# Optimization experiments

Hardware: AMD Instinct MI355X
Metric: run time of the kernel (lower is better)

The kernel has to match this reference:

```python
import jax, jax.numpy as jnp
import numpy as np

N_HEAD = 16
SPARSITY_K = 64


def _apply_rope(x):
    # x: [B, H, T, D]
    D = x.shape[-1]
    T = x.shape[-2]
    freqs = 1.0 / (10000.0 ** (jnp.arange(0, D, 2, dtype=jnp.float32) / D))  # [D/2]
    angles = jnp.arange(T, dtype=jnp.float32)[:, None] * freqs[None, :]      # [T, D/2]
    cos, sin = jnp.cos(angles), jnp.sin(angles)
    xe, xo = x[..., ::2], x[..., 1::2]
    re = xe * cos - xo * sin
    ro = xe * sin + xo * cos
    return jnp.stack([re, ro], axis=-1).reshape(x.shape)


def _sparse_mask(route_weights, T, k):
    # Per head h, per query t: keep positions j<=t whose route score is among
    # the top-k of route_weights[h, 0:t+1] (tie-break by smaller index, like topk).
    s = route_weights[:, :T]                      # [H, T]
    idx = jnp.arange(T)
    # G[h, jp, j] = 1 if position jp beats position j in the top-k ordering
    G = (s[:, :, None] > s[:, None, :]) | ((s[:, :, None] == s[:, None, :]) & (idx[:, None] < idx[None, :]))
    rank = jnp.cumsum(G.astype(jnp.int32), axis=1)  # rank[h, t, j] = #{jp<=t beating j}
    causal = idx[None, :, None] >= idx[None, None, :]  # j <= t
    return causal & (rank < k)                    # [H, T, T] bool


def reference(x, W_attn, b_attn, W_proj, b_proj, route_weights):
    B, T, C = x.shape
    H = N_HEAD
    D = C // H
    qkv = x @ W_attn + b_attn                     # [B, T, 3C]
    q, k, v = jnp.split(qkv, 3, axis=-1)

    def heads(t):
        return t.reshape(B, T, H, D).transpose(0, 2, 1, 3)  # [B, H, T, D]

    q, k, v = heads(q), heads(k), heads(v)
    q = _apply_rope(q)
    k = _apply_rope(k)

    scores = jnp.einsum('bhtd,bhsd->bhts', q, k) / jnp.sqrt(jnp.float32(D))
    mask = _sparse_mask(route_weights, T, SPARSITY_K)       # [H, T, T]
    scores = jnp.where(mask[None], scores, -jnp.inf)
    attn = jax.nn.softmax(scores, axis=-1)                  # dropout off (eval mode)
    out = jnp.einsum('bhts,bhsd->bhtd', attn, v)
    out = out.transpose(0, 2, 1, 3).reshape(B, T, C)
    return out @ W_proj + b_proj


def setup_inputs() -> dict:
    key = jax.random.key(0)
    ks = jax.random.split(key, 6)
    B, T, C, H = 2, 2048, 2048, 16
    return {
        'x': jax.random.normal(ks[0], (B, T, C), dtype=jnp.float32),
        'W_attn': jax.random.normal(ks[1], (C, 3 * C), dtype=jnp.float32) * 0.02,
        'b_attn': jnp.zeros((3 * C,), dtype=jnp.float32),
        'W_proj': jax.random.normal(ks[2], (C, C), dtype=jnp.float32) * 0.02,
        'b_proj': jnp.zeros((C,), dtype=jnp.float32),
        'route_weights': jax.random.normal(ks[3], (H, T), dtype=jnp.float32) * 0.02,
    }
```

## Files before the change

### kernel.cpp

```cpp
#include <hip/hip_runtime.h>
#include <stdint.h>

#define B_ 2
#define T_ 2048
#define C_ 2048
#define H_ 16
#define D_ 128
#define KSP 64
#define C3 6144

typedef __attribute__((ext_vector_type(4))) float f32x4;
typedef __attribute__((ext_vector_type(8))) _Float16 f16x8;
typedef __attribute__((ext_vector_type(4))) _Float16 f16x4;
typedef __attribute__((ext_vector_type(2))) _Float16 f16x2;

__device__ __forceinline__ void gload16(const void* g, void* l) {
  __builtin_amdgcn_global_load_lds(
      (__attribute__((address_space(1))) void*)(uintptr_t)g,
      (__attribute__((address_space(3))) void*)(uint32_t)(uintptr_t)l,
      16, 0, 0);
}

__global__ void k_cvt(const float* __restrict__ in, _Float16* __restrict__ out, int n) {
  int i = (blockIdx.x * blockDim.x + threadIdx.x) * 4;
  if (i >= n) return;
  const float4 v = *(const float4*)(in + i);
  f16x4 o;
  o.x = (_Float16)v.x; o.y = (_Float16)v.y; o.z = (_Float16)v.z; o.w = (_Float16)v.w;
  *(f16x4*)(out + i) = o;
}

__global__ void k_tconv(const float* __restrict__ W, _Float16* __restrict__ WT, int K, int N) {
  __shared__ float tile[32][33];
  const int n0 = blockIdx.x * 32, k0 = blockIdx.y * 32;
  const int tx = threadIdx.x, ty = threadIdx.y;
#pragma unroll
  for (int r = 0; r < 4; ++r)
    tile[ty + r * 8][tx] = W[(size_t)(k0 + ty + r * 8) * N + n0 + tx];
  __syncthreads();
#pragma unroll
  for (int r = 0; r < 4; ++r)
    WT[(size_t)(n0 + ty + r * 8) * K + k0 + tx] = (_Float16)tile[tx][ty + r * 8];
}

template <int F16OUT, int NJ, int ROPE>
__global__ __launch_bounds__(512) void k_gemm256(const _Float16* __restrict__ A,
                                                 const _Float16* __restrict__ BT,
                                                 const float* __restrict__ bias,
                                                 void* __restrict__ Cout,
                                                 int M, int N, int K,
                                                 int RGC, int RH, int CW) {
  constexpr int BN = 64 * NJ;
  __shared__ __align__(16) _Float16 sA[2][256 * 64];
  __shared__ __align__(16) _Float16 sB[2][BN * 64];
  const int tid = threadIdx.x;
  const int lane = tid & 63;
  const int wid = tid >> 6;
  const int wr = wid >> 2;
  const int wc = wid & 3;
  const int lr = lane & 15;
  const int g = lane >> 4;
  const int rot = lr & 7;
  const int bid = blockIdx.x;
  const int x = bid & 7, q = bid >> 3;
  const int bm = (x / RGC) * RH + q / CW;
  const int bn = (x % RGC) * CW + q % CW;
  const size_t arow0 = (size_t)bm * 256;
  const size_t brow0 = (size_t)bn * BN;

  f32x4 acc[8][NJ];
#pragma unroll
  for (int mi = 0; mi < 8; ++mi)
#pragma unroll
    for (int nj = 0; nj < NJ; ++nj) acc[mi][nj] = (f32x4){0.f, 0.f, 0.f, 0.f};

  auto STAGE_A = [&](int slot, int k0) {
    const int rord[4] = {0, 2, 1, 3};
#pragma unroll
    for (int ri = 0; ri < 4; ++ri) {
      const int u = tid + rord[ri] * 512;
      const int row = u >> 3, grl = u & 7;
      const int grn = (grl - (row & 7)) & 7;
      gload16(A + (arow0 + row) * K + k0 + grn * 8, &sA[slot][u * 8]);
    }
  };
  auto STAGE_B = [&](int slot, int k0) {
#pragma unroll
    for (int r = 0; r < NJ; ++r) {
      const int u = tid + r * 512;
      const int row = u >> 3, grl = u & 7;
      const int grn = (grl - (row & 7)) & 7;
      gload16(BT + (brow0 + row) * K + k0 + grn * 8, &sB[slot][u * 8]);
    }
  };

  f16x8 af[4], bf[NJ];
  auto LDA = [&](int slot, int mh, int kk) {
#pragma unroll
    for (int mi = 0; mi < 4; ++mi) {
      const int row = wr * 128 + (mh * 4 + mi) * 16 + lr;
      af[mi] = *(const f16x8*)&sA[slot][row * 64 + (((kk * 4 + g + rot) & 7) << 3)];
    }
  };
  auto LDB = [&](int slot, int kk) {
#pragma unroll
    for (int nj = 0; nj < NJ; ++nj) {
      const int row = wc * (16 * NJ) + nj * 16 + lr;
      bf[nj] = *(const f16x8*)&sB[slot][row * 64 + (((kk * 4 + g + rot) & 7) << 3)];
    }
  };
  auto MFMAB = [&](int mh) {
    __builtin_amdgcn_s_setprio(1);
#pragma unroll
    for (int mi = 0; mi < 4; ++mi)
#pragma unroll
      for (int nj = 0; nj < NJ; ++nj)
        acc[mh * 4 + mi][nj] =
            __builtin_amdgcn_mfma_f32_16x16x32_f16(af[mi], bf[nj], acc[mh * 4 + mi][nj], 0, 0, 0);
    __builtin_amdgcn_s_setprio(0);
    __builtin_amdgcn_sched_barrier(0);
  };

  STAGE_B(0, 0);
  STAGE_A(0, 0);
  asm volatile("s_waitcnt vmcnt(2)" ::: "memory");
  __builtin_amdgcn_s_barrier();

  const int NT = K >> 6;
  for (int t = 0; t < NT; ++t) {
    const int s = t & 1, ns = s ^ 1;
    const bool pf = (t + 1 < NT);
    const int kn = (t + 1) << 6;
    LDB(s, 0);
    LDA(s, 0, 0);
    if (pf) STAGE_B(ns, kn);
    __builtin_amdgcn_s_barrier();
    asm volatile("s_waitcnt lgkmcnt(0)" ::: "memory");
    __builtin_amdgcn_sched_barrier(0);
    MFMAB(0);
    if (pf)
      asm volatile("s_waitcnt vmcnt(%0)" ::"i"(NJ) : "memory");
    else
      asm volatile("s_waitcnt vmcnt(0)" ::: "memory");
    __builtin_amdgcn_s_barrier();
    LDA(s, 1, 0);
    if (pf) STAGE_A(ns, kn);
    __builtin_amdgcn_s_barrier();
    asm volatile("s_waitcnt lgkmcnt(0)" ::: "memory");
    __builtin_amdgcn_sched_barrier(0);
    MFMAB(1);
    __builtin_amdgcn_s_barrier();
    LDB(s, 1);
    LDA(s, 0, 1);
    __builtin_amdgcn_s_barrier();
    asm volatile("s_waitcnt lgkmcnt(0)" ::: "memory");
    __builtin_amdgcn_sched_barrier(0);
    MFMAB(0);
    __builtin_amdgcn_s_barrier();
    LDA(s, 1, 1);
    __builtin_amdgcn_s_barrier();
    asm volatile("s_waitcnt lgkmcnt(0)" ::: "memory");
    __builtin_amdgcn_sched_barrier(0);
    MFMAB(1);
    if (pf)
      asm volatile("s_waitcnt vmcnt(2)" ::: "memory");
    __builtin_amdgcn_s_barrier();
  }
  const size_t row0 = arow0 + wr * 128;
  const size_t col0 = brow0 + wc * (16 * NJ);
  const float sgn = (lr & 1) ? 1.f : -1.f;
  const int t0 = ((int)(row0 & (T_ - 1))) + g * 4;
#pragma unroll
  for (int nj = 0; nj < NJ; ++nj) {
    const size_t colbase = col0 + nj * 16;
    const size_t col = colbase + lr;
    const float bv = bias[col];
    const bool dorope = ROPE && (colbase < 2 * C_);
    float c1 = 1.f, s1 = 0.f, c16 = 1.f, s16 = 0.f, cm = 1.f, sm = 0.f;
    if (dorope) {
      const float freq = __expf(-0.14391156831212787f * (float)(((int)col & 127) >> 1));
      __sincosf((float)t0 * freq, &sm, &cm);
      __sincosf(freq, &s1, &c1);
      __sincosf(16.f * freq, &s16, &c16);
    }
#pragma unroll
    for (int mi = 0; mi < 8; ++mi) {
      float cr = cm, sr = sm;
#pragma unroll
      for (int r = 0; r < 4; ++r) {
        const size_t row = row0 + mi * 16 + g * 4 + r;
        float v = acc[mi][nj][r] + bv;
        if (dorope) {
          const float pe = __shfl_xor(v, 1);
          v = v * cr + sgn * pe * sr;
          const float nc = cr * c1 - sr * s1;
          sr = sr * c1 + cr * s1;
          cr = nc;
        }
        if (F16OUT)
          ((_Float16*)Cout)[row * N + col] = (_Float16)v;
        else
          ((float*)Cout)[row * N + col] = v;
      }
      if (dorope) {
        const float nc = cm * c16 - sm * s16;
        sm = sm * c16 + cm * s16;
        cm = nc;
      }
    }
  }
}

__global__ __launch_bounds__(256) void k_death(const float* __restrict__ rw, int* __restrict__ dd) {
  const int widG = blockIdx.x * 4 + (threadIdx.x >> 6);
  const int lane = threadIdx.x & 63;
  const int h = widG >> 11, j = widG & (T_ - 1);
  const float* s = rw + h * T_;
  const float sj = s[j];
  int total = 0, d = T_;
  for (int base = 0; base < T_; base += 64) {
    const int t = base + lane;
    const float st = s[t];
    const bool beat = (st > sj) || (st == sj && t < j);
    const unsigned long long bal = __ballot(beat);
    const int c = __popcll(bal);
    if (total + c >= KSP) {
      const int need = KSP - total;
      const int p = __popcll(bal & ((1ull << lane) - 1ull));
      const unsigned long long win = __ballot(beat && (p == need - 1));
      d = base + __builtin_ctzll(win);
      break;
    }
    total += c;
  }
  if (lane == 0) dd[widG] = d;
}

__global__ __launch_bounds__(64) void k_slist(const int* __restrict__ dd,
                                              uint32_t* __restrict__ slist) {
  const int bid = blockIdx.x;
  const int qb = bid & 127, h = bid >> 7;
  const int i0 = qb * 16, i1 = i0 + 15;
  const int lane = threadIdx.x;
  const int* dh = dd + h * T_;
  uint32_t* lb = slist + (size_t)bid * 96;
  int total = 0;
  for (int base = 0; base <= i1; base += 64) {
    const int j = base + lane;
    const int dv = dh[j];
    const bool pred = (j <= i1) && (dv > i0);
    const unsigned long long bal = __ballot(pred);
    const int pos = total + __popcll(bal & ((1ull << lane) - 1ull));
    if (pred) lb[pos] = (uint32_t)j | ((uint32_t)dv << 12);
    total += __popcll(bal);
  }
  for (int s = total + lane; s < 96; s += 64) lb[s] = 0;
}

__global__ __launch_bounds__(64, 4) void k_mattn(const _Float16* __restrict__ qkv,
                                                 const uint32_t* __restrict__ slist,
                                                 _Float16* __restrict__ out) {
  __shared__ uint32_t jd[96];
  __shared__ int joff[96];
  __shared__ __align__(16) _Float16 Pl[16 * 104];
  __shared__ __align__(16) _Float16 VT[2048];
  const int bid = blockIdx.x;
  const int qb = bid & 127, h = (bid >> 7) & 15, b = bid >> 11;
  const int i0 = qb * 16;
  const int lane = threadIdx.x;
  const int g = lane >> 4, l = lane & 15;
  const uint32_t* lb = slist + (size_t)((h << 7) + qb) * 96;
  {
    const uint32_t pk = lb[lane];
    jd[lane] = pk;
    joff[lane] = (int)(pk & 0xFFFu) * C3;
    if (lane < 32) {
      const uint32_t pk1 = lb[64 + lane];
      jd[64 + lane] = pk1;
      joff[64 + lane] = (int)(pk1 & 0xFFFu) * C3;
    }
  }
  __syncthreads();
  const _Float16* qkvb = qkv + (size_t)b * T_ * C3;
  const _Float16* qrow = qkvb + (size_t)(i0 + l) * C3 + h * D_ + 8 * g;
  f16x8 bq[4];
#pragma unroll
  for (int c = 0; c < 4; ++c) bq[c] = *(const f16x8*)(qrow + 32 * c);
  f32x4 sacc[6];
  const _Float16* kbase = qkvb + C_ + h * D_ + 8 * g;
#pragma unroll
  for (int t = 0; t < 6; ++t) {
    const int jo = joff[16 * t + l];
    const _Float16* kr = kbase + jo;
    f16x8 ak[4];
#pragma unroll
    for (int c = 0; c < 4; ++c) ak[c] = *(const f16x8*)(kr + 32 * c);
    f32x4 a = {0.f, 0.f, 0.f, 0.f};
#pragma unroll
    for (int c = 0; c < 4; ++c)
      a = __builtin_amdgcn_mfma_f32_16x16x32_f16(ak[c], bq[c], a, 0, 0, 0);
    sacc[t] = a;
  }
  const int iq = i0 + l;
  float P[6][4];
  float m = -INFINITY;
#pragma unroll
  for (int t = 0; t < 6; ++t)
#pragma unroll
    for (int r = 0; r < 4; ++r) {
      const uint32_t pk = jd[16 * t + 4 * g + r];
      const int j = (int)(pk & 0xFFFu);
      const int d = (int)(pk >> 12);
      const bool ok = (j <= iq) && (d > iq);
      const float x = ok ? sacc[t][r] * 0.08838834764831845f : -INFINITY;
      P[t][r] = x;
      m = fmaxf(m, x);
    }
  m = fmaxf(m, __shfl_xor(m, 16));
  m = fmaxf(m, __shfl_xor(m, 32));
  float ssum = 0.f;
#pragma unroll
  for (int t = 0; t < 6; ++t)
#pragma unroll
    for (int r = 0; r < 4; ++r) {
      const float e = __expf(P[t][r] - m);
      P[t][r] = e;
      ssum += e;
    }
  ssum += __shfl_xor(ssum, 16);
  ssum += __shfl_xor(ssum, 32);
  const float inv = 1.0f / ssum;
#pragma unroll
  for (int t = 0; t < 6; ++t) {
    f16x4 w;
    w.x = (_Float16)(P[t][0] * inv);
    w.y = (_Float16)(P[t][1] * inv);
    w.z = (_Float16)(P[t][2] * inv);
    w.w = (_Float16)(P[t][3] * inv);
    *(f16x4*)&Pl[l * 104 + 16 * t + 4 * g] = w;
  }
  __syncthreads();
  f16x8 pf[3];
#pragma unroll
  for (int cc = 0; cc < 3; ++cc) pf[cc] = *(const f16x8*)&Pl[l * 104 + 32 * cc + 8 * g];
  f32x4 oacc[8];
#pragma unroll
  for (int mt = 0; mt < 8; ++mt) oacc[mt] = (f32x4){0.f, 0.f, 0.f, 0.f};
  const _Float16* vbase = qkvb + 2 * C_ + h * D_;
#pragma unroll
  for (int cc = 0; cc < 3; ++cc) {
    const int jo0 = joff[32 * cc + l];
    const int jo1 = joff[32 * cc + 16 + l];
#pragma unroll
    for (int dh = 0; dh < 2; ++dh) {
      f16x8 vl0[2], vl1[2];
#pragma unroll
      for (int cp = 0; cp < 2; ++cp) {
        vl0[cp] = *(const f16x8*)(vbase + jo0 + 64 * dh + 32 * cp + 8 * g);
        vl1[cp] = *(const f16x8*)(vbase + jo1 + 64 * dh + 32 * cp + 8 * g);
      }
      __syncthreads();
#pragma unroll
      for (int tau = 0; tau < 2; ++tau)
#pragma unroll
        for (int cp = 0; cp < 2; ++cp) {
          const int mtl = 2 * cp + (g >> 1);
          const int lt0 = 8 * (g & 1);
          const int gt = (2 * tau + (l >> 3)) ^ g;
          const int et = l & 7;
#pragma unroll
          for (int e = 0; e < 8; ++e) {
            const int idx = ((mtl * 16 + lt0 + e) * 4 + gt) * 8 + et;
            VT[idx] = tau ? vl1[cp][e] : vl0[cp][e];
          }
        }
      __syncthreads();
#pragma unroll
      for (int mtl = 0; mtl < 4; ++mtl) {
        const int sgr = (l >> 3) | ((mtl & 1) << 1);
        const f16x8 vf = *(const f16x8*)&VT[((mtl * 16 + l) * 4 + (g ^ sgr)) * 8];
        oacc[4 * dh + mtl] =
            __builtin_amdgcn_mfma_f32_16x16x32_f16(pf[cc], vf, oacc[4 * dh + mtl], 0, 0, 0);
      }
    }
  }
  _Float16* ob = out + (size_t)(b * T_ + i0 + 4 * g) * C_ + h * D_ + l;
#pragma unroll
  for (int mt = 0; mt < 8; ++mt)
#pragma unroll
    for (int r = 0; r < 4; ++r)
      ob[(size_t)r * C_ + 16 * mt] = (_Float16)oacc[mt][r];
}

extern "C" void kernel_launch(void* const* d_in, const int* in_sizes, int n_in,
                              void* d_out, int out_size, void* d_ws, size_t ws_size,
                              hipStream_t stream) {
  const float* x  = (const float*)d_in[0];
  const float* Wa = (const float*)d_in[1];
  const float* ba = (const float*)d_in[2];
  const float* Wp = (const float*)d_in[3];
  const float* bp = (const float*)d_in[4];
  const float* rw = (const float*)d_in[5];

  char* ws = (char*)d_ws;
  _Float16* qkv16 = (_Float16*)(ws);
  _Float16* WaT   = (_Float16*)(ws + (size_t)48 * 1024 * 1024);
  _Float16* WpT   = (_Float16*)(ws + (size_t)72 * 1024 * 1024);
  _Float16* x16   = (_Float16*)(ws + (size_t)80 * 1024 * 1024);
  int* dd  = (int*)(ws + (size_t)96 * 1024 * 1024);
  uint32_t* slist = (uint32_t*)(ws + (size_t)96 * 1024 * 1024 + (2 << 17));
  _Float16* att16 = x16;

  k_cvt<<<dim3((B_ * T_ * C_) / 1024), dim3(256), 0, stream>>>(x, x16, B_ * T_ * C_);
  k_tconv<<<dim3(C3 / 32, C_ / 32), dim3(32, 8), 0, stream>>>(Wa, WaT, C_, C3);
  k_tconv<<<dim3(C_ / 32, C_ / 32), dim3(32, 8), 0, stream>>>(Wp, WpT, C_, C_);
  k_gemm256<1, 3, 1><<<dim3(512), dim3(512), 0, stream>>>(
      x16, WaT, ba, (void*)qkv16, B_ * T_, C3, C_, 4, 8, 8);
  k_death<<<dim3(H_ * T_ / 4), dim3(256), 0, stream>>>(rw, dd);
  k_slist<<<dim3(H_ * (T_ / 16)), dim3(64), 0, stream>>>(dd, slist);
  k_mattn<<<dim3(B_ * H_ * (T_ / 16)), dim3(64), 0, stream>>>(qkv16, slist, att16);
  k_gemm256<0, 2, 0><<<dim3(256), dim3(512), 0, stream>>>(
      att16, WpT, bp, d_out, B_ * T_, C_, C_, 4, 8, 4);
}
```

Measured before the change: 244.5 us.

## Add 128x192-tile QKV GEMM kernel with fused RoPE, 1024 blocks

Introduces a new 256-thread GEMM kernel using 128x192 output tiles for the QKV projection, launched with 1024 blocks instead of 512 blocks of 256x192. The goal is better occupancy and CU load balance on the 256-CU device, at the cost of less operand reuse per tile. RoPE is fused into the new kernel's epilogue, and the old generic kernel's RoPE path is removed, so it now only handles the output projection with a simpler epilogue loop order.

```diff
diff --git a/kernel.cpp b/kernel.cpp
--- a/kernel.cpp
+++ b/kernel.cpp
@@ -41,6 +41,170 @@
 #pragma unroll
   for (int r = 0; r < 4; ++r)
     WT[(size_t)(n0 + ty + r * 8) * K + k0 + tx] = (_Float16)tile[tx][ty + r * 8];
+}
+
+__global__ __launch_bounds__(256) void k_gemm128(const _Float16* __restrict__ A,
+                                                 const _Float16* __restrict__ BT,
+                                                 const float* __restrict__ bias,
+                                                 _Float16* __restrict__ Cout,
+                                                 int M, int N, int K) {
+  constexpr int NJ = 6;
+  constexpr int BN = 192;
+  __shared__ __align__(16) _Float16 sA[2][128 * 64];
+  __shared__ __align__(16) _Float16 sB[2][BN * 64];
+  const int tid = threadIdx.x;
+  const int lane = tid & 63;
+  const int wid = tid >> 6;
+  const int wr = wid >> 1;
+  const int wc = wid & 1;
+  const int lr = lane & 15;
+  const int g = lane >> 4;
+  const int rot = lr & 7;
+  const int bid = blockIdx.x;
+  const int x = bid & 7, q = bid >> 3;
+  const int bm = (x >> 2) * 16 + (q >> 3);
+  const int bn = (x & 3) * 8 + (q & 7);
+  const size_t arow0 = (size_t)bm * 128;
+  const size_t brow0 = (size_t)bn * BN;
+
+  f32x4 acc[4][NJ];
+#pragma unroll
+  for (int mi = 0; mi < 4; ++mi)
+#pragma unroll
+    for (int nj = 0; nj < NJ; ++nj) acc[mi][nj] = (f32x4){0.f, 0.f, 0.f, 0.f};
+
+  auto STAGE_A = [&](int slot, int k0) {
+    const int rord[4] = {0, 2, 1, 3};
+#pragma unroll
+    for (int ri = 0; ri < 4; ++ri) {
+      const int u = tid + rord[ri] * 256;
+      const int row = u >> 3, grl = u & 7;
+      const int grn = (grl - (row & 7)) & 7;
+      gload16(A + (arow0 + row) * K + k0 + grn * 8, &sA[slot][u * 8]);
+    }
+  };
+  auto STAGE_B = [&](int slot, int k0) {
+#pragma unroll
+    for (int r = 0; r < NJ; ++r) {
+      const int u = tid + r * 256;
+      const int row = u >> 3, grl = u & 7;
+      const int grn = (grl - (row & 7)) & 7;
+      gload16(BT + (brow0 + row) * K + k0 + grn * 8, &sB[slot][u * 8]);
+    }
+  };
+
+  f16x8 af[2], bf[NJ];
+  auto LDA = [&](int slot, int mh, int kk) {
+#pragma unroll
+    for (int mi = 0; mi < 2; ++mi) {
+      const int row = wr * 64 + (mh * 2 + mi) * 16 + lr;
+      af[mi] = *(const f16x8*)&sA[slot][row * 64 + (((kk * 4 + g + rot) & 7) << 3)];
+    }
+  };
+  auto LDB = [&](int slot, int kk) {
+#pragma unroll
+    for (int nj = 0; nj < NJ; ++nj) {
+      const int row = wc * 96 + nj * 16 + lr;
+      bf[nj] = *(const f16x8*)&sB[slot][row * 64 + (((kk * 4 + g + rot) & 7) << 3)];
+    }
+  };
+  auto MFMAB = [&](int mh) {
+    __builtin_amdgcn_s_setprio(1);
+#pragma unroll
+    for (int mi = 0; mi < 2; ++mi)
+#pragma unroll
+      for (int nj = 0; nj < NJ; ++nj)
+        acc[mh * 2 + mi][nj] =
+            __builtin_amdgcn_mfma_f32_16x16x32_f16(af[mi], bf[nj], acc[mh * 2 + mi][nj], 0, 0, 0);
+    __builtin_amdgcn_s_setprio(0);
+    __builtin_amdgcn_sched_barrier(0);
+  };
+
+  STAGE_B(0, 0);
+  STAGE_A(0, 0);
+  asm volatile("s_waitcnt vmcnt(2)" ::: "memory");
+  __builtin_amdgcn_s_barrier();
+
+  const int NT = K >> 6;
+  for (int t = 0; t < NT; ++t) {
+    const int s = t & 1, ns = s ^ 1;
+    const bool pf = (t + 1 < NT);
+    const int kn = (t + 1) << 6;
+    LDB(s, 0);
+    LDA(s, 0, 0);
+    if (pf) STAGE_B(ns, kn);
+    __builtin_amdgcn_s_barrier();
+    asm volatile("s_waitcnt lgkmcnt(0)" ::: "memory");
+    __builtin_amdgcn_sched_barrier(0);
+    MFMAB(0);
+    if (pf)
+      asm volatile("s_waitcnt vmcnt(%0)" ::"i"(NJ) : "memory");
+    else
+      asm volatile("s_waitcnt vmcnt(0)" ::: "memory");
+    __builtin_amdgcn_s_barrier();
+    LDA(s, 1, 0);
+    if (pf) STAGE_A(ns, kn);
+    __builtin_amdgcn_s_barrier();
+    asm volatile("s_waitcnt lgkmcnt(0)" ::: "memory");
+    __builtin_amdgcn_sched_barrier(0);
+    MFMAB(1);
+    __builtin_amdgcn_s_barrier();
+    LDB(s, 1);
+    LDA(s, 0, 1);
+    __builtin_amdgcn_s_barrier();
+    asm volatile("s_waitcnt lgkmcnt(0)" ::: "memory");
+    __builtin_amdgcn_sched_barrier(0);
+    MFMAB(0);
+    __builtin_amdgcn_s_barrier();
+    LDA(s, 1, 1);
+    __builtin_amdgcn_s_barrier();
+    asm volatile("s_waitcnt lgkmcnt(0)" ::: "memory");
+    __builtin_amdgcn_sched_barrier(0);
+    MFMAB(1);
+    if (pf)
+      asm volatile("s_waitcnt vmcnt(2)" ::: "memory");
+    __builtin_amdgcn_s_barrier();
+  }
+  const size_t row0 = arow0 + wr * 64;
+  const size_t col0 = brow0 + wc * 96;
+  const float sgn = (lr & 1) ? 1.f : -1.f;
+  const int t0 = ((int)(row0 & (T_ - 1))) + g * 4;
+#pragma unroll
+  for (int nj = 0; nj < NJ; ++nj) {
+    const size_t colbase = col0 + nj * 16;
+    const size_t col = colbase + lr;
+    const float bv = bias[col];
+    const bool dorope = colbase < 2 * C_;
+    float c1 = 1.f, s1 = 0.f, c16 = 1.f, s16 = 0.f, cm = 1.f, sm = 0.f;
+    if (dorope) {
+      const float freq = __expf(-0.14391156831212787f * (float)(((int)col & 127) >> 1));
+      __sincosf((float)t0 * freq, &sm, &cm);
+      __sincosf(freq, &s1, &c1);
+      __sincosf(16.f * freq, &s16, &c16);
+    }
+#pragma unroll
+    for (int mi = 0; mi < 4; ++mi) {
+      float cr = cm, sr = sm;
+#pragma unroll
+      for (int r = 0; r < 4; ++r) {
+        const size_t row = row0 + mi * 16 + g * 4 + r;
+        float v = acc[mi][nj][r] + bv;
+        if (dorope) {
+          const float pe = __shfl_xor(v, 1);
+          v = v * cr + sgn * pe * sr;
+          const float nc = cr * c1 - sr * s1;
+          sr = sr * c1 + cr * s1;
+          cr = nc;
+        }
+        Cout[row * N + col] = (_Float16)v;
+      }
+      if (dorope) {
+        const float nc = cm * c16 - sm * s16;
+        sm = sm * c16 + cm * s16;
+        cm = nc;
+      }
+    }
+  }
 }
 
 template <int F16OUT, int NJ, int ROPE>
@@ -168,44 +332,20 @@
   }
   const size_t row0 = arow0 + wr * 128;
   const size_t col0 = brow0 + wc * (16 * NJ);
-  const float sgn = (lr & 1) ? 1.f : -1.f;
-  const int t0 = ((int)(row0 & (T_ - 1))) + g * 4;
-#pragma unroll
-  for (int nj = 0; nj < NJ; ++nj) {
-    const size_t colbase = col0 + nj * 16;
-    const size_t col = colbase + lr;
-    const float bv = bias[col];
-    const bool dorope = ROPE && (colbase < 2 * C_);
-    float c1 = 1.f, s1 = 0.f, c16 = 1.f, s16 = 0.f, cm = 1.f, sm = 0.f;
-    if (dorope) {
-      const float freq = __expf(-0.14391156831212787f * (float)(((int)col & 127) >> 1));
-      __sincosf((float)t0 * freq, &sm, &cm);
-      __sincosf(freq, &s1, &c1);
-      __sincosf(16.f * freq, &s16, &c16);
-    }
-#pragma unroll
-    for (int mi = 0; mi < 8; ++mi) {
-      float cr = cm, sr = sm;
+#pragma unroll
+  for (int mi = 0; mi < 8; ++mi) {
+#pragma unroll
+    for (int nj = 0; nj < NJ; ++nj) {
+      const size_t col = col0 + nj * 16 + lr;
+      const float bv = bias[col];
 #pragma unroll
       for (int r = 0; r < 4; ++r) {
         const size_t row = row0 + mi * 16 + g * 4 + r;
-        float v = acc[mi][nj][r] + bv;
-        if (dorope) {
-          const float pe = __shfl_xor(v, 1);
-          v = v * cr + sgn * pe * sr;
-          const float nc = cr * c1 - sr * s1;
-          sr = sr * c1 + cr * s1;
-          cr = nc;
-        }
+        const float v = acc[mi][nj][r] + bv;
         if (F16OUT)
           ((_Float16*)Cout)[row * N + col] = (_Float16)v;
         else
           ((float*)Cout)[row * N + col] = v;
-      }
-      if (dorope) {
-        const float nc = cm * c16 - sm * s16;
-        sm = sm * c16 + cm * s16;
-        cm = nc;
       }
     }
   }
@@ -414,8 +554,8 @@
   k_cvt<<<dim3((B_ * T_ * C_) / 1024), dim3(256), 0, stream>>>(x, x16, B_ * T_ * C_);
   k_tconv<<<dim3(C3 / 32, C_ / 32), dim3(32, 8), 0, stream>>>(Wa, WaT, C_, C3);
   k_tconv<<<dim3(C_ / 32, C_ / 32), dim3(32, 8), 0, stream>>>(Wp, WpT, C_, C_);
-  k_gemm256<1, 3, 1><<<dim3(512), dim3(512), 0, stream>>>(
-      x16, WaT, ba, (void*)qkv16, B_ * T_, C3, C_, 4, 8, 8);
+  k_gemm128<<<dim3(1024), dim3(256), 0, stream>>>(
+      x16, WaT, ba, qkv16, B_ * T_, C3, C_);
   k_death<<<dim3(H_ * T_ / 4), dim3(256), 0, stream>>>(rw, dd);
   k_slist<<<dim3(H_ * (T_ / 16)), dim3(64), 0, stream>>>(dd, slist);
   k_mattn<<<dim3(B_ * H_ * (T_ / 16)), dim3(64), 0, stream>>>(qkv16, slist, att16);
```

After: 302.1 us. +23.6%, slower.
